# Performance work log

Measured on AMD Instinct MI355X. Metric: run time of the kernel, lower is better.

## Reference

```python
import jax, jax.numpy as jnp
import numpy as np

NUM_CODES = 512
CODE_DIM = 64
COMMITMENT_COST = 0.1
DECAY = 0.9
EPS = 1e-5


def setup_inputs() -> dict:
    key = jax.random.key(0)
    k1, k2, k3 = jax.random.split(key, 3)
    B, L, D, K = 32, 4096, CODE_DIM, NUM_CODES
    z_e = jax.random.normal(k1, (B, L, D), dtype=jnp.float32)
    emb = jax.random.uniform(k2, (K, D), dtype=jnp.float32, minval=-1.0 / K, maxval=1.0 / K)
    ema_cluster_size = jnp.ones((K,), dtype=jnp.float32)
    ema_w = emb + 0.01 * jax.random.normal(k3, (K, D), dtype=jnp.float32)
    return {"z_e": z_e, "emb": emb, "ema_cluster_size": ema_cluster_size, "ema_w": ema_w}


def reference(z_e, emb, ema_cluster_size, ema_w):
    B, L, D = z_e.shape
    K = emb.shape[0]
    flat = z_e.reshape(-1, D)                                   # [N, D]
    dists = (jnp.sum(flat * flat, axis=1, keepdims=True)
             - 2.0 * flat @ emb.T
             + jnp.sum(emb * emb, axis=1)[None, :])
    codes = jnp.argmin(dists, axis=1)                           # [N] int
    z_q = emb[codes].reshape(B, L, D)
    # straight-through estimator
    z_q_st = z_e + jax.lax.stop_gradient(z_q - z_e)
    # EMA updates (training, no_grad) via direct scatter-reduce instead of one-hot matmul
    cluster_size = jax.ops.segment_sum(jnp.ones_like(codes, dtype=z_e.dtype), codes, num_segments=K)
    new_ecs = ema_cluster_size * DECAY + cluster_size * (1.0 - DECAY)
    dw = jax.ops.segment_sum(flat, codes, num_segments=K)       # [K, D]
    new_ema_w = ema_w * DECAY + dw * (1.0 - DECAY)
    n = jnp.sum(new_ecs)
    cs_smoothed = (new_ecs + EPS) / (n + K * EPS) * n
    new_emb = new_ema_w / (cs_smoothed[:, None] + EPS)
    # commitment loss (z_q detached)
    commit = jnp.mean((z_e - jax.lax.stop_gradient(z_q)) ** 2)
    loss_vq = COMMITMENT_COST * commit
    return (z_q_st, loss_vq, codes.reshape(B, L), new_ecs, new_ema_w, new_emb)
```

## Files before the change

kernel.cpp:

```cpp
#include <hip/hip_runtime.h>
#include <math.h>

#define NROWS 131072
#define DIM 64
#define NCODE 512
#define FLAG_CAP 32768

#define OUT_ZQ    0
#define OUT_LOSS  8388608
#define OUT_CODES 8388609
#define OUT_ECS   8519681
#define OUT_EMAW  8520193
#define OUT_EMB   8552961

#define WS_LOSS    0
#define WS_N       8
#define WS_FLAGC   12
#define WS_COUNTS  16
#define WS_OFFSETS 2064
#define WS_CURSOR  4112
#define WS_CSUM    6160
#define WS_EHI     8208
#define WS_ELO     73744
#define WS_CODESI  139280
#define WS_DW4     139280
#define WS_BUCKET  663568
#define WS_FLAGR   663568
#define WS_BYTES   1187856
#define WS_ZERO_BYTES 2064

#define DECAY_C ((float)0.9)
#define OMD_C   ((float)(1.0 - 0.9))
#define EPS_C   ((float)1e-5)

typedef float f32x4 __attribute__((ext_vector_type(4)));
typedef short short8v __attribute__((ext_vector_type(8)));

__device__ __forceinline__ unsigned short bf16_rne_bits(float f) {
    unsigned int u = __float_as_uint(f);
    unsigned int r = u + 0x7fffu + ((u >> 16) & 1u);
    return (unsigned short)(r >> 16);
}

__device__ __forceinline__ float np_pairwise64_sq(const float* v) {
    float r[8];
#pragma unroll
    for (int j = 0; j < 8; ++j) r[j] = __fmul_rn(v[j], v[j]);
#pragma unroll
    for (int b = 1; b < 8; ++b) {
#pragma unroll
        for (int j = 0; j < 8; ++j)
            r[j] = __fadd_rn(r[j], __fmul_rn(v[8 * b + j], v[8 * b + j]));
    }
    return __fadd_rn(__fadd_rn(__fadd_rn(r[0], r[1]), __fadd_rn(r[2], r[3])),
                     __fadd_rn(__fadd_rn(r[4], r[5]), __fadd_rn(r[6], r[7])));
}

__global__ void k_csum(const float* __restrict__ emb, float* __restrict__ csum) {
    int k = blockIdx.x * blockDim.x + threadIdx.x;
    if (k >= NCODE) return;
    float e[DIM];
#pragma unroll
    for (int d = 0; d < DIM; d += 4) {
        float4 v = *reinterpret_cast<const float4*>(emb + (size_t)k * DIM + d);
        e[d] = v.x; e[d + 1] = v.y; e[d + 2] = v.z; e[d + 3] = v.w;
    }
    csum[k] = np_pairwise64_sq(e);
}

__global__ __launch_bounds__(256) void k_split(
        const float* __restrict__ emb, unsigned short* __restrict__ ehi,
        unsigned short* __restrict__ elo) {
    int i = blockIdx.x * 256 + threadIdx.x;
    if (i >= NCODE * DIM) return;
    float v = emb[i];
    unsigned short h = bf16_rne_bits(v);
    float hf = __uint_as_float((unsigned int)h << 16);
    ehi[i] = h;
    elo[i] = bf16_rne_bits(v - hf);
}

#define CVTE(H, L, j, val) { \
    unsigned int ub = __float_as_uint(val); \
    unsigned int rr = ub + 0x7fffu + ((ub >> 16) & 1u); \
    unsigned short hb = (unsigned short)(rr >> 16); \
    float hf2 = __uint_as_float(((unsigned int)hb) << 16); \
    float lof = (val) - hf2; \
    unsigned int ul = __float_as_uint(lof); \
    unsigned int rl = ul + 0x7fffu + ((ul >> 16) & 1u); \
    H[j] = (short)hb; L[j] = (short)(rl >> 16); }

__global__ __launch_bounds__(256, 1) void k_mfma(
        const float* __restrict__ ze, const float* __restrict__ emb,
        const unsigned short* __restrict__ ehi, const unsigned short* __restrict__ elo,
        const float* __restrict__ csum, float* __restrict__ out,
        int* __restrict__ codes_i, int* __restrict__ counts,
        double* __restrict__ lossAcc, int* __restrict__ flagC, int* __restrict__ flagR) {
    __shared__ float cs[NCODE];
    __shared__ int h[NCODE];
    __shared__ float A_s[128];
    __shared__ int code_s[128];
    __shared__ double ls[4];
    int tid = threadIdx.x;
    for (int i = tid; i < NCODE; i += 256) { cs[i] = csum[i]; h[i] = 0; }
    if (tid < 128) {
        const float* xr = ze + (size_t)(blockIdx.x * 128 + tid) * DIM;
        float xv[DIM];
#pragma unroll
        for (int d = 0; d < DIM; d += 4) {
            float4 v = *reinterpret_cast<const float4*>(xr + d);
            xv[d] = v.x; xv[d + 1] = v.y; xv[d + 2] = v.z; xv[d + 3] = v.w;
        }
        A_s[tid] = np_pairwise64_sq(xv);
    }
    __syncthreads();

    int wid = tid >> 6;
    int lane = tid & 63;
    int r16 = lane & 15;
    int kg = lane >> 4;
    int rowbase = blockIdx.x * 128 + wid * 32;

    float Ar[2][4];
#pragma unroll
    for (int rt = 0; rt < 2; ++rt)
#pragma unroll
        for (int reg = 0; reg < 4; ++reg)
            Ar[rt][reg] = A_s[wid * 32 + rt * 16 + 4 * kg + reg];

    short8v ahi[2][2], alo[2][2];
#define LOADA(rt, hf) { \
        const float4* ap = reinterpret_cast<const float4*>( \
            ze + (size_t)(rowbase + (rt) * 16 + r16) * DIM + (hf) * 32 + 8 * kg); \
        float4 u = ap[0], w = ap[1]; \
        CVTE(ahi[rt][hf], alo[rt][hf], 0, u.x) CVTE(ahi[rt][hf], alo[rt][hf], 1, u.y) \
        CVTE(ahi[rt][hf], alo[rt][hf], 2, u.z) CVTE(ahi[rt][hf], alo[rt][hf], 3, u.w) \
        CVTE(ahi[rt][hf], alo[rt][hf], 4, w.x) CVTE(ahi[rt][hf], alo[rt][hf], 5, w.y) \
        CVTE(ahi[rt][hf], alo[rt][hf], 6, w.z) CVTE(ahi[rt][hf], alo[rt][hf], 7, w.w) }
    LOADA(0, 0) LOADA(0, 1) LOADA(1, 0) LOADA(1, 1)

    float m1v[2][4], m2v[2][4];
    int i1v[2][4];
#pragma unroll
    for (int rt = 0; rt < 2; ++rt)
#pragma unroll
        for (int j = 0; j < 4; ++j) { m1v[rt][j] = 3.4e38f; m2v[rt][j] = 3.4e38f; i1v[rt][j] = 0; }

#define UPD(C, rt, reg) { \
        float u = __fsub_rn(Ar[rt][reg], __fadd_rn(C[reg], C[reg])); \
        float s = __fadd_rn(u, csv); \
        if (s < m1v[rt][reg]) { m2v[rt][reg] = m1v[rt][reg]; m1v[rt][reg] = s; i1v[rt][reg] = codeIdx; } \
        else if (s < m2v[rt][reg]) { m2v[rt][reg] = s; } }

    for (int t = 0; t < 32; ++t) {
        const short8v* bh = reinterpret_cast<const short8v*>(
            ehi + (size_t)(t * 16 + r16) * DIM + 8 * kg);
        const short8v* bl = reinterpret_cast<const short8v*>(
            elo + (size_t)(t * 16 + r16) * DIM + 8 * kg);
        short8v bh0 = bh[0], bh1 = bh[4];
        short8v bl0 = bl[0], bl1 = bl[4];
        f32x4 c0 = {0.f, 0.f, 0.f, 0.f};
        f32x4 c1 = {0.f, 0.f, 0.f, 0.f};
        c0 = __builtin_amdgcn_mfma_f32_16x16x32_bf16(ahi[0][0], bh0, c0, 0, 0, 0);
        c0 = __builtin_amdgcn_mfma_f32_16x16x32_bf16(ahi[0][1], bh1, c0, 0, 0, 0);
        c0 = __builtin_amdgcn_mfma_f32_16x16x32_bf16(alo[0][0], bh0, c0, 0, 0, 0);
        c0 = __builtin_amdgcn_mfma_f32_16x16x32_bf16(alo[0][1], bh1, c0, 0, 0, 0);
        c0 = __builtin_amdgcn_mfma_f32_16x16x32_bf16(ahi[0][0], bl0, c0, 0, 0, 0);
        c0 = __builtin_amdgcn_mfma_f32_16x16x32_bf16(ahi[0][1], bl1, c0, 0, 0, 0);
        c1 = __builtin_amdgcn_mfma_f32_16x16x32_bf16(ahi[1][0], bh0, c1, 0, 0, 0);
        c1 = __builtin_amdgcn_mfma_f32_16x16x32_bf16(ahi[1][1], bh1, c1, 0, 0, 0);
        c1 = __builtin_amdgcn_mfma_f32_16x16x32_bf16(alo[1][0], bh0, c1, 0, 0, 0);
        c1 = __builtin_amdgcn_mfma_f32_16x16x32_bf16(alo[1][1], bh1, c1, 0, 0, 0);
        c1 = __builtin_amdgcn_mfma_f32_16x16x32_bf16(ahi[1][0], bl0, c1, 0, 0, 0);
        c1 = __builtin_amdgcn_mfma_f32_16x16x32_bf16(ahi[1][1], bl1, c1, 0, 0, 0);
        float csv = cs[t * 16 + r16];
        int codeIdx = t * 16 + r16;
        UPD(c0, 0, 0) UPD(c0, 0, 1) UPD(c0, 0, 2) UPD(c0, 0, 3)
        UPD(c1, 1, 0) UPD(c1, 1, 1) UPD(c1, 1, 2) UPD(c1, 1, 3)
    }

#define RED(rt, reg, mask) { \
        float om1 = __shfl_xor(m1v[rt][reg], mask); \
        int   oi  = __shfl_xor(i1v[rt][reg], mask); \
        float om2 = __shfl_xor(m2v[rt][reg], mask); \
        if (om1 < m1v[rt][reg]) { \
            m2v[rt][reg] = fminf(m1v[rt][reg], om2); m1v[rt][reg] = om1; i1v[rt][reg] = oi; \
        } else if (om1 > m1v[rt][reg]) { \
            m2v[rt][reg] = fminf(m2v[rt][reg], om1); \
        } else { \
            if (oi < i1v[rt][reg]) i1v[rt][reg] = oi; \
            m2v[rt][reg] = m1v[rt][reg]; } }
#define RED4(rt, reg) RED(rt, reg, 1) RED(rt, reg, 2) RED(rt, reg, 4) RED(rt, reg, 8)
    RED4(0, 0) RED4(0, 1) RED4(0, 2) RED4(0, 3)
    RED4(1, 0) RED4(1, 1) RED4(1, 2) RED4(1, 3)

    if (r16 == 0) {
#define WOUT(rt, reg) { \
        int lrow = wid * 32 + (rt) * 16 + 4 * kg + (reg); \
        int row = blockIdx.x * 128 + lrow; \
        code_s[lrow] = i1v[rt][reg]; \
        out[OUT_CODES + row] = (float)i1v[rt][reg]; \
        codes_i[row] = i1v[rt][reg]; \
        atomicAdd(&h[i1v[rt][reg]], 1); \
        if (m2v[rt][reg] - m1v[rt][reg] < Ar[rt][reg] * 6e-7f) { \
            int pos = atomicAdd(flagC, 1); \
            if (pos < FLAG_CAP) flagR[pos] = row; } }
        WOUT(0, 0) WOUT(0, 1) WOUT(0, 2) WOUT(0, 3)
        WOUT(1, 0) WOUT(1, 1) WOUT(1, 2) WOUT(1, 3)
    }
    __syncthreads();

    double lpart = 0.0;
#pragma unroll 4
    for (int r = 0; r < 32; ++r) {
        int code = code_s[wid * 32 + r];
        int row = rowbase + r;
        float x = ze[(size_t)row * DIM + lane];
        float e = emb[(size_t)code * DIM + lane];
        float tdiff = __fsub_rn(e, x);
        out[OUT_ZQ + (size_t)row * DIM + lane] = __fadd_rn(x, tdiff);
        lpart += (double)tdiff * tdiff;
    }
    for (int off = 32; off; off >>= 1) lpart += __shfl_down(lpart, off);
    if (lane == 0) ls[wid] = lpart;
    __syncthreads();
    if (tid == 0) atomicAdd(lossAcc, (ls[0] + ls[1]) + (ls[2] + ls[3]));
    for (int k = tid; k < NCODE; k += 256) {
        int cc = h[k];
        if (cc) atomicAdd(&counts[k], cc);
    }
}

__global__ __launch_bounds__(64) void k_rescue(
        const float* __restrict__ ze, const float* __restrict__ emb,
        const float* __restrict__ csum, float* __restrict__ out,
        int* __restrict__ codes_i, int* __restrict__ counts,
        double* __restrict__ lossAcc, const int* __restrict__ flagC,
        const int* __restrict__ flagR) {
    __shared__ float x2s[DIM];
    int nf = *flagC;
    if (nf > FLAG_CAP) nf = FLAG_CAP;
    int lane = threadIdx.x;
    for (int i = blockIdx.x; i < nf; i += gridDim.x) {
        int row = flagR[i];
        __syncthreads();
        float v = ze[(size_t)row * DIM + lane];
        x2s[lane] = __fadd_rn(v, v);
        __syncthreads();
        float r[8];
#pragma unroll
        for (int j = 0; j < 8; ++j) r[j] = __fmul_rn(x2s[j], x2s[j]);
#pragma unroll
        for (int b = 1; b < 8; ++b) {
#pragma unroll
            for (int j = 0; j < 8; ++j)
                r[j] = __fadd_rn(r[j], __fmul_rn(x2s[8 * b + j], x2s[8 * b + j]));
        }
        float A = __fmul_rn(0.25f,
            __fadd_rn(__fadd_rn(__fadd_rn(r[0], r[1]), __fadd_rn(r[2], r[3])),
                      __fadd_rn(__fadd_rn(r[4], r[5]), __fadd_rn(r[6], r[7]))));
        float m1 = 3.4e38f;
        int i1 = 0x7fffffff;
#pragma unroll
        for (int kk = 0; kk < 8; ++kk) {
            int k = lane * 8 + kk;
            const float* e = emb + (size_t)k * DIM;
            float a = 0.f;
#pragma unroll
            for (int d = 0; d < DIM; ++d) a = __builtin_fmaf(x2s[d], e[d], a);
            float t = __fadd_rn(__fsub_rn(A, a), csum[k]);
            if (t < m1) { m1 = t; i1 = k; }
        }
        for (int off = 32; off; off >>= 1) {
            float ov = __shfl_xor(m1, off);
            int oi = __shfl_xor(i1, off);
            if (ov < m1 || (ov == m1 && oi < i1)) { m1 = ov; i1 = oi; }
        }
        int oldc = codes_i[row];
        if (i1 != oldc) {
            if (lane == 0) {
                codes_i[row] = i1;
                out[OUT_CODES + row] = (float)i1;
                atomicSub(&counts[oldc], 1);
                atomicAdd(&counts[i1], 1);
            }
            float x = __fmul_rn(0.5f, x2s[lane]);
            float en = emb[(size_t)i1 * DIM + lane];
            float eo = emb[(size_t)oldc * DIM + lane];
            float tn = __fsub_rn(en, x);
            float to = __fsub_rn(eo, x);
            out[OUT_ZQ + (size_t)row * DIM + lane] = __fadd_rn(x, tn);
            double dl = (double)tn * tn - (double)to * to;
            for (int off = 32; off; off >>= 1) dl += __shfl_down(dl, off);
            if (lane == 0) atomicAdd(lossAcc, dl);
        }
    }
}

__global__ __launch_bounds__(512) void k_scan(
        const int* __restrict__ counts, int* __restrict__ offsets, int* __restrict__ cursor,
        const float* __restrict__ ecs_in, float* __restrict__ out, float* __restrict__ n_out) {
    __shared__ int sa[NCODE], sb[NCODE];
    __shared__ float red[NCODE];
    int k = threadIdx.x;
    int c = counts[k];
    sa[k] = c;
    float v = __fadd_rn(__fmul_rn(ecs_in[k], DECAY_C), __fmul_rn((float)c, OMD_C));
    out[OUT_ECS + k] = v;
    red[k] = v;
    __syncthreads();
    int* src = sa;
    int* dst = sb;
    for (int off = 1; off < NCODE; off <<= 1) {
        dst[k] = (k >= off) ? src[k - off] + src[k] : src[k];
        __syncthreads();
        int* tp = src; src = dst; dst = tp;
    }
    offsets[k] = src[k] - c;
    cursor[k]  = src[k] - c;
    for (int s = NCODE / 2; s > 0; s >>= 1) {
        if (k < s) red[k] += red[k + s];
        __syncthreads();
    }
    if (k == 0) n_out[0] = red[0];
}

__global__ __launch_bounds__(256) void k_scatter(
        const int* __restrict__ codes_i, int* __restrict__ cursor, int* __restrict__ bucket) {
    int row = blockIdx.x * 256 + threadIdx.x;
    int c = codes_i[row];
    int pos = atomicAdd(&cursor[c], 1);
    bucket[pos] = row;
}

__global__ __launch_bounds__(256) void k_dw(
        const float* __restrict__ ze, const int* __restrict__ bucket,
        const int* __restrict__ offsets, const int* __restrict__ counts,
        float* __restrict__ dw4) {
    __shared__ float p[4][DIM];
    int k = blockIdx.x >> 2;
    int q = blockIdx.x & 3;
    int w = threadIdx.x >> 6;
    int d = threadIdx.x & 63;
    int s = offsets[k];
    int n = counts[k];
    float acc0 = 0.f, acc1 = 0.f;
    int i = q + 4 * w;
    for (; i + 16 < n; i += 32) {
        int ra = bucket[s + i];
        int rb = bucket[s + i + 16];
        acc0 += ze[(size_t)ra * DIM + d];
        acc1 += ze[(size_t)rb * DIM + d];
    }
    if (i < n) acc0 += ze[(size_t)bucket[s + i] * DIM + d];
    p[w][d] = acc0 + acc1;
    __syncthreads();
    if (w == 0) dw4[((size_t)q * NCODE + k) * DIM + d] = (p[0][d] + p[1][d]) + (p[2][d] + p[3][d]);
}

__global__ __launch_bounds__(256) void k_final(
        const float* __restrict__ ema_w, const float* __restrict__ dw4,
        const float* __restrict__ n_ptr, const double* __restrict__ lossAcc,
        float* __restrict__ out) {
    int i = blockIdx.x * blockDim.x + threadIdx.x;
    if (i >= NCODE * DIM) return;
    int k = i >> 6;
    float dsum = __fadd_rn(__fadd_rn(dw4[i], dw4[i + NCODE * DIM]),
                           __fadd_rn(dw4[i + 2 * NCODE * DIM], dw4[i + 3 * NCODE * DIM]));
    float w = __fadd_rn(__fmul_rn(ema_w[i], DECAY_C), __fmul_rn(dsum, OMD_C));
    out[OUT_EMAW + i] = w;
    float n = n_ptr[0];
    float necs = out[OUT_ECS + k];
    float cs = (necs + EPS_C) / (n + (float)NCODE * EPS_C) * n;
    out[OUT_EMB + i] = w / (cs + EPS_C);
    if (i == 0) out[OUT_LOSS] = (float)(0.1 * (lossAcc[0] / (double)((size_t)NROWS * DIM)));
}

extern "C" void kernel_launch(void* const* d_in, const int* in_sizes, int n_in,
                              void* d_out, int out_size, void* d_ws, size_t ws_size,
                              hipStream_t stream) {
    const float* ze   = (const float*)d_in[0];
    const float* emb  = (const float*)d_in[1];
    const float* ecs  = (const float*)d_in[2];
    const float* emaw = (const float*)d_in[3];
    float* out = (float*)d_out;
    char* ws = (char*)d_ws;
    double* lossAcc = (double*)(ws + WS_LOSS);
    float*  n_out   = (float*)(ws + WS_N);
    int*    flagC   = (int*)(ws + WS_FLAGC);
    int*    counts  = (int*)(ws + WS_COUNTS);
    int*    offsets = (int*)(ws + WS_OFFSETS);
    int*    cursor  = (int*)(ws + WS_CURSOR);
    float*  csum    = (float*)(ws + WS_CSUM);
    unsigned short* ehi = (unsigned short*)(ws + WS_EHI);
    unsigned short* elo = (unsigned short*)(ws + WS_ELO);
    int*    codes_i = (int*)(ws + WS_CODESI);
    float*  dw4     = (float*)(ws + WS_DW4);
    int*    bucket  = (int*)(ws + WS_BUCKET);
    int*    flagR   = (int*)(ws + WS_FLAGR);

    hipMemsetAsync(d_ws, 0, WS_ZERO_BYTES, stream);
    hipLaunchKernelGGL(k_csum, dim3(2), dim3(256), 0, stream, emb, csum);
    hipLaunchKernelGGL(k_split, dim3(NCODE * DIM / 256), dim3(256), 0, stream, emb, ehi, elo);
    hipLaunchKernelGGL(k_mfma, dim3(NROWS / 128), dim3(256), 0, stream,
                       ze, emb, ehi, elo, csum, out, codes_i, counts, lossAcc, flagC, flagR);
    hipLaunchKernelGGL(k_rescue, dim3(2048), dim3(64), 0, stream,
                       ze, emb, csum, out, codes_i, counts, lossAcc, flagC, flagR);
    hipLaunchKernelGGL(k_scan, dim3(1), dim3(512), 0, stream,
                       counts, offsets, cursor, ecs, out, n_out);
    hipLaunchKernelGGL(k_scatter, dim3(NROWS / 256), dim3(256), 0, stream,
                       codes_i, cursor, bucket);
    hipLaunchKernelGGL(k_dw, dim3(NCODE * 4), dim3(256), 0, stream,
                       ze, bucket, offsets, counts, dw4);
    hipLaunchKernelGGL(k_final, dim3(NCODE * DIM / 256), dim3(256), 0, stream,
                       emaw, dw4, n_out, lossAcc, out);
}
```

Before: 216.7 us.

## Fuse workspace zeroing and bf16 split into csum kernel; split MFMA accumulation chains

Drops the memset and the separate k_split launch by folding counter zeroing and the hi/lo bf16 split of the codebook into k_csum, removing two launches. The MFMA loop now uses two independent accumulators per row tile, so the dependent MFMA chain is half as long and more instructions can be in flight, with the halves summed before the distance update. The split work now runs on only 512 threads doing strided 2-byte stores. The different accumulation order could change which code wins a near-tie.

```diff
diff --git a/kernel.cpp b/kernel.cpp
--- a/kernel.cpp
+++ b/kernel.cpp
@@ -27,7 +27,6 @@
 #define WS_BUCKET  663568
 #define WS_FLAGR   663568
 #define WS_BYTES   1187856
-#define WS_ZERO_BYTES 2064
 
 #define DECAY_C ((float)0.9)
 #define OMD_C   ((float)(1.0 - 0.9))
@@ -56,9 +55,14 @@
                      __fadd_rn(__fadd_rn(r[4], r[5]), __fadd_rn(r[6], r[7])));
 }
 
-__global__ void k_csum(const float* __restrict__ emb, float* __restrict__ csum) {
+__global__ void k_csum(const float* __restrict__ emb, float* __restrict__ csum,
+                       unsigned short* __restrict__ ehi, unsigned short* __restrict__ elo,
+                       int* __restrict__ counts, int* __restrict__ flagC,
+                       double* __restrict__ lossAcc, float* __restrict__ n_out) {
     int k = blockIdx.x * blockDim.x + threadIdx.x;
     if (k >= NCODE) return;
+    counts[k] = 0;
+    if (k == 0) { *flagC = 0; *lossAcc = 0.0; *n_out = 0.f; }
     float e[DIM];
 #pragma unroll
     for (int d = 0; d < DIM; d += 4) {
@@ -66,18 +70,13 @@
         e[d] = v.x; e[d + 1] = v.y; e[d + 2] = v.z; e[d + 3] = v.w;
     }
     csum[k] = np_pairwise64_sq(e);
-}
-
-__global__ __launch_bounds__(256) void k_split(
-        const float* __restrict__ emb, unsigned short* __restrict__ ehi,
-        unsigned short* __restrict__ elo) {
-    int i = blockIdx.x * 256 + threadIdx.x;
-    if (i >= NCODE * DIM) return;
-    float v = emb[i];
-    unsigned short h = bf16_rne_bits(v);
-    float hf = __uint_as_float((unsigned int)h << 16);
-    ehi[i] = h;
-    elo[i] = bf16_rne_bits(v - hf);
+#pragma unroll
+    for (int d = 0; d < DIM; ++d) {
+        unsigned short hb = bf16_rne_bits(e[d]);
+        float hf = __uint_as_float((unsigned int)hb << 16);
+        ehi[k * DIM + d] = hb;
+        elo[k * DIM + d] = bf16_rne_bits(e[d] - hf);
+    }
 }
 
 #define CVTE(H, L, j, val) { \
@@ -146,8 +145,9 @@
 #pragma unroll
         for (int j = 0; j < 4; ++j) { m1v[rt][j] = 3.4e38f; m2v[rt][j] = 3.4e38f; i1v[rt][j] = 0; }
 
-#define UPD(C, rt, reg) { \
-        float u = __fsub_rn(Ar[rt][reg], __fadd_rn(C[reg], C[reg])); \
+#define UPD(CA, CB, rt, reg) { \
+        float dsum = __fadd_rn(CA[reg], CB[reg]); \
+        float u = __fsub_rn(Ar[rt][reg], __fadd_rn(dsum, dsum)); \
         float s = __fadd_rn(u, csv); \
         if (s < m1v[rt][reg]) { m2v[rt][reg] = m1v[rt][reg]; m1v[rt][reg] = s; i1v[rt][reg] = codeIdx; } \
         else if (s < m2v[rt][reg]) { m2v[rt][reg] = s; } }
@@ -159,24 +159,24 @@
             elo + (size_t)(t * 16 + r16) * DIM + 8 * kg);
         short8v bh0 = bh[0], bh1 = bh[4];
         short8v bl0 = bl[0], bl1 = bl[4];
-        f32x4 c0 = {0.f, 0.f, 0.f, 0.f};
-        f32x4 c1 = {0.f, 0.f, 0.f, 0.f};
-        c0 = __builtin_amdgcn_mfma_f32_16x16x32_bf16(ahi[0][0], bh0, c0, 0, 0, 0);
-        c0 = __builtin_amdgcn_mfma_f32_16x16x32_bf16(ahi[0][1], bh1, c0, 0, 0, 0);
-        c0 = __builtin_amdgcn_mfma_f32_16x16x32_bf16(alo[0][0], bh0, c0, 0, 0, 0);
-        c0 = __builtin_amdgcn_mfma_f32_16x16x32_bf16(alo[0][1], bh1, c0, 0, 0, 0);
-        c0 = __builtin_amdgcn_mfma_f32_16x16x32_bf16(ahi[0][0], bl0, c0, 0, 0, 0);
-        c0 = __builtin_amdgcn_mfma_f32_16x16x32_bf16(ahi[0][1], bl1, c0, 0, 0, 0);
-        c1 = __builtin_amdgcn_mfma_f32_16x16x32_bf16(ahi[1][0], bh0, c1, 0, 0, 0);
-        c1 = __builtin_amdgcn_mfma_f32_16x16x32_bf16(ahi[1][1], bh1, c1, 0, 0, 0);
-        c1 = __builtin_amdgcn_mfma_f32_16x16x32_bf16(alo[1][0], bh0, c1, 0, 0, 0);
-        c1 = __builtin_amdgcn_mfma_f32_16x16x32_bf16(alo[1][1], bh1, c1, 0, 0, 0);
-        c1 = __builtin_amdgcn_mfma_f32_16x16x32_bf16(ahi[1][0], bl0, c1, 0, 0, 0);
-        c1 = __builtin_amdgcn_mfma_f32_16x16x32_bf16(ahi[1][1], bl1, c1, 0, 0, 0);
+        f32x4 c0a = {0.f, 0.f, 0.f, 0.f}, c0b = {0.f, 0.f, 0.f, 0.f};
+        f32x4 c1a = {0.f, 0.f, 0.f, 0.f}, c1b = {0.f, 0.f, 0.f, 0.f};
+        c0a = __builtin_amdgcn_mfma_f32_16x16x32_bf16(ahi[0][0], bh0, c0a, 0, 0, 0);
+        c0b = __builtin_amdgcn_mfma_f32_16x16x32_bf16(ahi[0][1], bh1, c0b, 0, 0, 0);
+        c1a = __builtin_amdgcn_mfma_f32_16x16x32_bf16(ahi[1][0], bh0, c1a, 0, 0, 0);
+        c1b = __builtin_amdgcn_mfma_f32_16x16x32_bf16(ahi[1][1], bh1, c1b, 0, 0, 0);
+        c0a = __builtin_amdgcn_mfma_f32_16x16x32_bf16(alo[0][0], bh0, c0a, 0, 0, 0);
+        c0b = __builtin_amdgcn_mfma_f32_16x16x32_bf16(alo[0][1], bh1, c0b, 0, 0, 0);
+        c1a = __builtin_amdgcn_mfma_f32_16x16x32_bf16(alo[1][0], bh0, c1a, 0, 0, 0);
+        c1b = __builtin_amdgcn_mfma_f32_16x16x32_bf16(alo[1][1], bh1, c1b, 0, 0, 0);
+        c0a = __builtin_amdgcn_mfma_f32_16x16x32_bf16(ahi[0][0], bl0, c0a, 0, 0, 0);
+        c0b = __builtin_amdgcn_mfma_f32_16x16x32_bf16(ahi[0][1], bl1, c0b, 0, 0, 0);
+        c1a = __builtin_amdgcn_mfma_f32_16x16x32_bf16(ahi[1][0], bl0, c1a, 0, 0, 0);
+        c1b = __builtin_amdgcn_mfma_f32_16x16x32_bf16(ahi[1][1], bl1, c1b, 0, 0, 0);
         float csv = cs[t * 16 + r16];
         int codeIdx = t * 16 + r16;
-        UPD(c0, 0, 0) UPD(c0, 0, 1) UPD(c0, 0, 2) UPD(c0, 0, 3)
-        UPD(c1, 1, 0) UPD(c1, 1, 1) UPD(c1, 1, 2) UPD(c1, 1, 3)
+        UPD(c0a, c0b, 0, 0) UPD(c0a, c0b, 0, 1) UPD(c0a, c0b, 0, 2) UPD(c0a, c0b, 0, 3)
+        UPD(c1a, c1b, 1, 0) UPD(c1a, c1b, 1, 1) UPD(c1a, c1b, 1, 2) UPD(c1a, c1b, 1, 3)
     }
 
 #define RED(rt, reg, mask) { \
@@ -399,9 +399,8 @@
     int*    bucket  = (int*)(ws + WS_BUCKET);
     int*    flagR   = (int*)(ws + WS_FLAGR);
 
-    hipMemsetAsync(d_ws, 0, WS_ZERO_BYTES, stream);
-    hipLaunchKernelGGL(k_csum, dim3(2), dim3(256), 0, stream, emb, csum);
-    hipLaunchKernelGGL(k_split, dim3(NCODE * DIM / 256), dim3(256), 0, stream, emb, ehi, elo);
+    hipLaunchKernelGGL(k_csum, dim3(2), dim3(256), 0, stream,
+                       emb, csum, ehi, elo, counts, flagC, lossAcc, n_out);
     hipLaunchKernelGGL(k_mfma, dim3(NROWS / 128), dim3(256), 0, stream,
                        ze, emb, ehi, elo, csum, out, codes_i, counts, lossAcc, flagC, flagR);
     hipLaunchKernelGGL(k_rescue, dim3(2048), dim3(64), 0, stream,
```

After: 239.1 us. 10.3% more time.
